# Kernel optimization log

Measured on AMD Instinct MI355X. Metric: run time of the kernel, lower is better.

The kernel has to match this reference:

```python
import jax, jax.numpy as jnp
import numpy as np

B = 16384
DIM = 1024
HEADS = 16
LN_EPS = 1e-5


def setup_inputs() -> dict:
    key = jax.random.key(0)
    ks = jax.random.split(key, 8)
    d = DIM
    s = 0.02
    return {
        "x_u": jax.random.normal(ks[0], (B, d), dtype=jnp.float32),
        "x_m": jax.random.normal(ks[1], (B, d), dtype=jnp.float32),
        # MHA m2u (path 1): packed in_proj [3d, d] like torch, out_proj [d, d]
        "w_qkv1": (jax.random.normal(ks[2], (3 * d, d), dtype=jnp.float32) * s),
        "b_qkv1": jnp.zeros((3 * d,), dtype=jnp.float32),
        "w_o1": (jax.random.normal(ks[3], (d, d), dtype=jnp.float32) * s),
        "b_o1": jnp.zeros((d,), dtype=jnp.float32),
        # MHA u2m (path 2)
        "w_qkv2": (jax.random.normal(ks[4], (3 * d, d), dtype=jnp.float32) * s),
        "b_qkv2": jnp.zeros((3 * d,), dtype=jnp.float32),
        "w_o2": (jax.random.normal(ks[5], (d, d), dtype=jnp.float32) * s),
        "b_o2": jnp.zeros((d,), dtype=jnp.float32),
        # proj head: LayerNorm(2d) + Linear(2d -> d) + GELU (dropout = eval identity)
        "ln_g": jnp.ones((2 * d,), dtype=jnp.float32),
        "ln_b": jnp.zeros((2 * d,), dtype=jnp.float32),
        "w_proj": (jax.random.normal(ks[6], (d, 2 * d), dtype=jnp.float32) * s),
        "b_proj": jnp.zeros((d,), dtype=jnp.float32),
        "heads": HEADS,
    }


def _mha_single_token(xq, xkv, w_qkv, b_qkv, w_o, b_o, heads):
    # seq_len = 1 cross-attention: softmax over a single key is exactly 1.
    d = xq.shape[-1]
    dh = d // heads
    wq, wk, wv = jnp.split(w_qkv, 3, axis=0)
    bq, bk, bv = jnp.split(b_qkv, 3)
    q = (xq @ wq.T + bq).reshape(-1, heads, dh)   # [B, H, dh]
    k = (xkv @ wk.T + bk).reshape(-1, heads, dh)
    v = (xkv @ wv.T + bv).reshape(-1, heads, dh)
    scores = jnp.sum(q * k, axis=-1) / jnp.sqrt(jnp.asarray(dh, q.dtype))  # [B, H]
    attn = jax.nn.softmax(scores[..., None], axis=-1)  # singleton key axis -> ones
    out = (attn * v).reshape(-1, d)                    # [B, d]
    return out @ w_o.T + b_o


def reference(x_u, x_m, w_qkv1, b_qkv1, w_o1, b_o1,
              w_qkv2, b_qkv2, w_o2, b_o2,
              ln_g, ln_b, w_proj, b_proj, heads):
    # Path 1: Q = x_m, K/V = x_u ; Path 2: Q = x_u, K/V = x_m
    z1 = _mha_single_token(x_m, x_u, w_qkv1, b_qkv1, w_o1, b_o1, heads)
    z2 = _mha_single_token(x_u, x_m, w_qkv2, b_qkv2, w_o2, b_o2, heads)
    z = jnp.concatenate([z1, z2], axis=-1)  # [B, 2d]
    mu = jnp.mean(z, axis=-1, keepdims=True)
    var = jnp.mean(jnp.square(z - mu), axis=-1, keepdims=True)
    zn = (z - mu) * jax.lax.rsqrt(var + LN_EPS) * ln_g + ln_b
    h = zn @ w_proj.T + b_proj               # [B, d]
    return jax.nn.gelu(h, approximate=False)  # torch nn.GELU default = exact erf
```

## Files before the change

kernel.cpp:

```cpp
#include <hip/hip_runtime.h>
#include <cstdint>


#define DIM 1024
#define BROWS 16384

typedef __bf16 bf16x8 __attribute__((ext_vector_type(8)));
typedef float f32x4 __attribute__((ext_vector_type(4)));

__device__ __forceinline__ ushort f2bf(float f) {
    uint32_t u = __builtin_bit_cast(uint32_t, f);
    u = (u + 0x7fffu + ((u >> 16) & 1u)) >> 16;
    return (ushort)u;
}

__device__ __forceinline__ void async_copy16(const void* gsrc, void* ldst) {
    __builtin_amdgcn_global_load_lds(
        (__attribute__((address_space(1))) void*)((uintptr_t)gsrc),
        (__attribute__((address_space(3))) void*)((uint32_t)(uintptr_t)ldst),
        16, 0, 0);
}


__global__ __launch_bounds__(256) void prep_kernel(
        const float* __restrict__ x_u, const float* __restrict__ x_m,
        const float* __restrict__ wqkv1, const float* __restrict__ bqkv1,
        const float* __restrict__ wo1, const float* __restrict__ bo1,
        const float* __restrict__ wqkv2, const float* __restrict__ bqkv2,
        const float* __restrict__ wo2, const float* __restrict__ bo2,
        const float* __restrict__ lng, const float* __restrict__ lnb,
        const float* __restrict__ wproj, const float* __restrict__ bproj,
        ushort* __restrict__ x_bf, ushort* __restrict__ wo12,
        ushort* __restrict__ wvT12, ushort* __restrict__ Wp,
        float* __restrict__ b12, float* __restrict__ Svec, float* __restrict__ Cvec,
        float* __restrict__ sums ) {
    const int b = blockIdx.x, t = threadIdx.x;
    __shared__ float red[4][4];
    __shared__ float tls[32][33];

    if (b < 8192) {
        const int n4 = (BROWS * DIM) / 4;
        int i = b * 256 + t;
        const int stride = 8192 * 256;
        const float4* xu4 = (const float4*)x_u;
        const float4* xm4 = (const float4*)x_m;
        ushort4* o4 = (ushort4*)x_bf;
#pragma unroll
        for (int it = 0; it < 4; it++, i += stride) {
            float4 v = (i < n4) ? xu4[i] : xm4[i - n4];
            ushort4 o;
            o.x = f2bf(v.x); o.y = f2bf(v.y); o.z = f2bf(v.z); o.w = f2bf(v.w);
            o4[i] = o;
        }
    } else if (b < 9216) {
        int j = b - 8192;
        float s1 = 0.f, s2 = 0.f, sS = 0.f, sC = 0.f;
        for (int c = t; c < DIM; c += 256) {
            s1 += wo1[j * DIM + c] * bqkv1[2 * DIM + c];
            s2 += wo2[j * DIM + c] * bqkv2[2 * DIM + c];
        }
        for (int c = t; c < 2 * DIM; c += 256) {
            float w = wproj[j * 2 * DIM + c];
            sS += w * lng[c];
            sC += w * lnb[c];
        }
        for (int o = 32; o; o >>= 1) {
            s1 += __shfl_down(s1, o, 64);
            s2 += __shfl_down(s2, o, 64);
            sS += __shfl_down(sS, o, 64);
            sC += __shfl_down(sC, o, 64);
        }
        int wid = t >> 6;
        if ((t & 63) == 0) { red[wid][0] = s1; red[wid][1] = s2; red[wid][2] = sS; red[wid][3] = sC; }
        __syncthreads();
        if (t == 0) {
            s1 = red[0][0] + red[1][0] + red[2][0] + red[3][0];
            s2 = red[0][1] + red[1][1] + red[2][1] + red[3][1];
            sS = red[0][2] + red[1][2] + red[2][2] + red[3][2];
            sC = red[0][3] + red[1][3] + red[2][3] + red[3][3];
            b12[j]       = s1 + bo1[j];
            b12[DIM + j] = s2 + bo2[j];
            Svec[j] = sS;
            Cvec[j] = sC + bproj[j];
        }
    } else if (b < 12288) {
        const int NWO = (DIM * DIM) / 4;
        const int NWP = (DIM * 2 * DIM) / 4;
        const int total = 2 * NWO + NWP;
        int i = (b - 9216) * 256 + t;
        const int stride = 3072 * 256;
        for (; i < total; i += stride) {
            if (i < 2 * NWO) {
                float4 v = (i < NWO) ? ((const float4*)wo1)[i] : ((const float4*)wo2)[i - NWO];
                ushort4 o;
                o.x = f2bf(v.x); o.y = f2bf(v.y); o.z = f2bf(v.z); o.w = f2bf(v.w);
                ((ushort4*)wo12)[i] = o;
            } else {
                int j = i - 2 * NWO;
                float4 v = ((const float4*)wproj)[j];
                int c = (j * 4) & (2 * DIM - 1);
                v.x *= lng[c]; v.y *= lng[c + 1]; v.z *= lng[c + 2]; v.w *= lng[c + 3];
                ushort4 o;
                o.x = f2bf(v.x); o.y = f2bf(v.y); o.z = f2bf(v.z); o.w = f2bf(v.w);
                ((ushort4*)Wp)[j] = o;
            }
        }
    } else if (b < 14336) {
        int tile = b - 12288;
        int z = tile >> 10;
        int t2 = tile & 1023;
        int mt = t2 >> 5, kt = t2 & 31;
        const float* src = z ? wqkv2 : wqkv1;
        int tr = t >> 3;
        int tc4 = (t & 7) * 4;
        const float* p = src + (long)(2 * DIM + mt * 32 + tr) * DIM + kt * 32 + tc4;
        float4 v = *(const float4*)p;
        tls[tr][tc4 + 0] = v.x; tls[tr][tc4 + 1] = v.y;
        tls[tr][tc4 + 2] = v.z; tls[tr][tc4 + 3] = v.w;
        __syncthreads();
        ushort4 o;
        o.x = f2bf(tls[tc4 + 0][tr]);
        o.y = f2bf(tls[tc4 + 1][tr]);
        o.z = f2bf(tls[tc4 + 2][tr]);
        o.w = f2bf(tls[tc4 + 3][tr]);
        *(ushort4*)(wvT12 + (long)z * DIM * DIM + (long)(kt * 32 + tr) * DIM + mt * 32 + tc4) = o;
    } else {
        int i = (b - 14336) * 256 + t;
        ((float4*)sums)[i] = float4{0.f, 0.f, 0.f, 0.f};
    }
}

template <int BM, int BN, int MODE>
__global__ __launch_bounds__(256, 2) void gemm_bt(
        const ushort* __restrict__ Ag, const ushort* __restrict__ Wg,
        void* __restrict__ Cg, int K, int lda, int ldw, int ldc,
        long sAz, long sWz, long sCz,
        const float* __restrict__ bias,
        const float* __restrict__ Svec, const float* __restrict__ Cvec,
        float* __restrict__ sumbuf, float* __restrict__ sqbuf) {
    constexpr int BK = 32;
    constexpr int MT = BM / 32;
    constexpr int NT = BN / 32;
    __shared__ __align__(16) ushort As[BM * BK];
    __shared__ __align__(16) ushort Bs[BN * BK];
    const int tid = threadIdx.x;
    const int wid = tid >> 6;
    const int lane = tid & 63;
    const int quad = lane >> 4;
    const int l16 = lane & 15;
    const int waveM = wid >> 1, waveN = wid & 1;
    const int zb = blockIdx.z;

    const ushort* A = Ag + zb * sAz + (long)blockIdx.x * BM * lda;
    const ushort* W = Wg + zb * sWz + (long)blockIdx.y * BN * ldw;

    f32x4 acc[MT][NT] = {};

    constexpr int nA = (BM * BK) / (256 * 8);
    constexpr int nB = (BN * BK) / (256 * 8);

    const int swz = (l16 >> 1) & 3;
    const int rdA = quad ^ swz;
    for (int k0 = 0; k0 < K; k0 += BK) {
#pragma unroll
        for (int c = 0; c < nA; c++) {
            int idx = c * 256 + tid;
            int r = idx >> 2;
            int q = (idx & 3) ^ ((r >> 1) & 3);
            const ushort* g = A + (long)r * lda + k0 + q * 8;
            async_copy16(g, (char*)As + (c * 256 + wid * 64) * 16);
        }
#pragma unroll
        for (int c = 0; c < nB; c++) {
            int idx = c * 256 + tid;
            int r = idx >> 2;
            int q = (idx & 3) ^ ((r >> 1) & 3);
            const ushort* g = W + (long)r * ldw + k0 + q * 8;
            async_copy16(g, (char*)Bs + (c * 256 + wid * 64) * 16);
        }
        asm volatile("s_waitcnt vmcnt(0)" ::: "memory");
        __syncthreads();

        bf16x8 af[MT], bfg[NT];
#pragma unroll
        for (int im = 0; im < MT; im++)
            af[im] = *(const bf16x8*)(As + (waveM * (BM / 2) + im * 16 + l16) * BK + rdA * 8);
#pragma unroll
        for (int in = 0; in < NT; in++)
            bfg[in] = *(const bf16x8*)(Bs + (waveN * (BN / 2) + in * 16 + l16) * BK + rdA * 8);
#pragma unroll
        for (int im = 0; im < MT; im++)
#pragma unroll
            for (int in = 0; in < NT; in++)
                acc[im][in] = __builtin_amdgcn_mfma_f32_16x16x32_bf16(
                    af[im], bfg[in], acc[im][in], 0, 0, 0);
        __syncthreads();
    }

    const int gRow0 = blockIdx.x * BM + waveM * (BM / 2) + quad * 4;
    const int gCol0 = blockIdx.y * BN + waveN * (BN / 2) + l16;
    if constexpr (MODE == 0) {
        ushort* C = (ushort*)Cg + zb * sCz;
#pragma unroll
        for (int im = 0; im < MT; im++)
#pragma unroll
            for (int in = 0; in < NT; in++) {
                int col = gCol0 + in * 16;
#pragma unroll
                for (int r = 0; r < 4; r++) {
                    int row = gRow0 + im * 16 + r;
                    C[(long)row * ldc + col] = f2bf(acc[im][in][r]);
                }
            }
    } else if constexpr (MODE == 1) {
        ushort* C = (ushort*)Cg + zb * sCz;
        float rs[MT][4] = {};
        float rq[MT][4] = {};
#pragma unroll
        for (int im = 0; im < MT; im++)
#pragma unroll
            for (int in = 0; in < NT; in++) {
                int col = gCol0 + in * 16;
                float badd = bias[zb * DIM + col];
#pragma unroll
                for (int r = 0; r < 4; r++) {
                    int row = gRow0 + im * 16 + r;
                    float val = acc[im][in][r] + badd;
                    C[(long)row * ldc + col] = f2bf(val);
                    rs[im][r] += val;
                    rq[im][r] += val * val;
                }
            }
#pragma unroll
        for (int im = 0; im < MT; im++)
#pragma unroll
            for (int r = 0; r < 4; r++) {
                float s = rs[im][r], q = rq[im][r];
#pragma unroll
                for (int o = 1; o < 16; o <<= 1) {
                    s += __shfl_xor(s, o, 64);
                    q += __shfl_xor(q, o, 64);
                }
                if (l16 == 0) {
                    int row = gRow0 + im * 16 + r;
                    atomicAdd(&sumbuf[row], s);
                    atomicAdd(&sqbuf[row], q);
                }
            }
    } else {
        float* O = (float*)Cg;
#pragma unroll
        for (int im = 0; im < MT; im++)
#pragma unroll
            for (int r = 0; r < 4; r++) {
                int row = gRow0 + im * 16 + r;
                float sv = sumbuf[row], qv = sqbuf[row];
                float m = sv * (1.f / 2048.f);
                float var = qv * (1.f / 2048.f) - m * m;
                float rstd = rsqrtf(var + 1e-5f);
#pragma unroll
                for (int in = 0; in < NT; in++) {
                    int col = gCol0 + in * 16;
                    float h = rstd * (acc[im][in][r] - m * Svec[col]) + Cvec[col];
                    O[(long)row * ldc + col] = 0.5f * h * (1.0f + erff(h * 0.7071067811865475f));
                }
            }
    }
}


extern "C" void kernel_launch(void* const* d_in, const int* in_sizes, int n_in,
                              void* d_out, int out_size, void* d_ws, size_t ws_size,
                              hipStream_t stream) {
    (void)in_sizes; (void)n_in; (void)out_size; (void)ws_size;
    const float* x_u   = (const float*)d_in[0];
    const float* x_m   = (const float*)d_in[1];
    const float* wqkv1 = (const float*)d_in[2];
    const float* bqkv1 = (const float*)d_in[3];
    const float* wo1   = (const float*)d_in[4];
    const float* bo1   = (const float*)d_in[5];
    const float* wqkv2 = (const float*)d_in[6];
    const float* bqkv2 = (const float*)d_in[7];
    const float* wo2   = (const float*)d_in[8];
    const float* bo2   = (const float*)d_in[9];
    const float* lng   = (const float*)d_in[10];
    const float* lnb   = (const float*)d_in[11];
    const float* wproj = (const float*)d_in[12];
    const float* bproj = (const float*)d_in[13];

    char* ws = (char*)d_ws;
    ushort* x_bf  = (ushort*)(ws + 0);
    ushort* wo12  = (ushort*)(ws + 67108864);
    ushort* wvT12 = (ushort*)(ws + 71303168);
    ushort* W12   = (ushort*)(ws + 75497472);
    ushort* Wp    = (ushort*)(ws + 79691776);
    ushort* zbuf  = (ushort*)(ws + 83886080);
    float*  b12   = (float*)(ws + 150994944);
    float*  Svec  = (float*)(ws + 151003136);
    float*  Cvec  = (float*)(ws + 151007232);
    float*  sumbuf= (float*)(ws + 151011328);
    float*  sqbuf = (float*)(ws + 151076864);

    prep_kernel<<<14368, 256, 0, stream>>>(
        x_u, x_m, wqkv1, bqkv1, wo1, bo1, wqkv2, bqkv2, wo2, bo2,
        lng, lnb, wproj, bproj,
        x_bf, wo12, wvT12, Wp, b12, Svec, Cvec, sumbuf);

    gemm_bt<64, 64, 0><<<dim3(16, 16, 2), 256, 0, stream>>>(
        wo12, wvT12, W12, DIM, DIM, DIM, DIM,
        (long)DIM * DIM, (long)DIM * DIM, (long)DIM * DIM,
        nullptr, nullptr, nullptr, nullptr, nullptr);

    gemm_bt<128, 128, 1><<<dim3(128, 8, 2), 256, 0, stream>>>(
        x_bf, W12, zbuf, DIM, DIM, DIM, 2 * DIM,
        (long)BROWS * DIM, (long)DIM * DIM, (long)DIM,
        b12, nullptr, nullptr, sumbuf, sqbuf);

    gemm_bt<128, 128, 2><<<dim3(128, 8, 1), 256, 0, stream>>>(
        zbuf, Wp, d_out, 2 * DIM, 2 * DIM, 2 * DIM, DIM,
        0, 0, 0,
        nullptr, Svec, Cvec, sumbuf, sqbuf);
}
```

Baseline: 408.0 us.

## Use 256x256 tiled GEMM with 4-stage async LDS pipeline for main GEMMs

Replaces the 128x128 single-buffered GEMM for the two big matmuls with a 512-thread 256x256 tile kernel. It uses a 4-deep LDS ring buffer filled by async global-to-LDS copies, with partial vmcnt waits, so loads overlap MFMA compute. It also adds s_setprio around the MFMA bursts. The larger tile raises data reuse per block but uses 128KB of LDS and many accumulator registers, which limits occupancy. The grid also shrinks to 512 blocks, which may leave some CUs idle in the tail.

```diff
diff --git a/kernel.cpp b/kernel.cpp
--- a/kernel.cpp
+++ b/kernel.cpp
@@ -20,7 +20,6 @@
         (__attribute__((address_space(3))) void*)((uint32_t)(uintptr_t)ldst),
         16, 0, 0);
 }
-
 
 __global__ __launch_bounds__(256) void prep_kernel(
         const float* __restrict__ x_u, const float* __restrict__ x_m,
@@ -33,7 +32,7 @@
         ushort* __restrict__ x_bf, ushort* __restrict__ wo12,
         ushort* __restrict__ wvT12, ushort* __restrict__ Wp,
         float* __restrict__ b12, float* __restrict__ Svec, float* __restrict__ Cvec,
-        float* __restrict__ sums ) {
+        float* __restrict__ sums) {
     const int b = blockIdx.x, t = threadIdx.x;
     __shared__ float red[4][4];
     __shared__ float tls[32][33];
@@ -130,15 +129,11 @@
     }
 }
 
-template <int BM, int BN, int MODE>
-__global__ __launch_bounds__(256, 2) void gemm_bt(
+__global__ __launch_bounds__(256, 2) void gemm_w(
         const ushort* __restrict__ Ag, const ushort* __restrict__ Wg,
-        void* __restrict__ Cg, int K, int lda, int ldw, int ldc,
-        long sAz, long sWz, long sCz,
-        const float* __restrict__ bias,
-        const float* __restrict__ Svec, const float* __restrict__ Cvec,
-        float* __restrict__ sumbuf, float* __restrict__ sqbuf) {
-    constexpr int BK = 32;
+        ushort* __restrict__ Cg, int K, int lda, int ldw, int ldc,
+        long sAz, long sWz, long sCz) {
+    constexpr int BM = 64, BN = 64, BK = 32;
     constexpr int MT = BM / 32;
     constexpr int NT = BN / 32;
     __shared__ __align__(16) ushort As[BM * BK];
@@ -155,10 +150,8 @@
     const ushort* W = Wg + zb * sWz + (long)blockIdx.y * BN * ldw;
 
     f32x4 acc[MT][NT] = {};
-
     constexpr int nA = (BM * BK) / (256 * 8);
     constexpr int nB = (BN * BK) / (256 * 8);
-
     const int swz = (l16 >> 1) & 3;
     const int rdA = quad ^ swz;
     for (int k0 = 0; k0 < K; k0 += BK) {
@@ -167,16 +160,14 @@
             int idx = c * 256 + tid;
             int r = idx >> 2;
             int q = (idx & 3) ^ ((r >> 1) & 3);
-            const ushort* g = A + (long)r * lda + k0 + q * 8;
-            async_copy16(g, (char*)As + (c * 256 + wid * 64) * 16);
+            async_copy16(A + (long)r * lda + k0 + q * 8, (char*)As + (c * 256 + wid * 64) * 16);
         }
 #pragma unroll
         for (int c = 0; c < nB; c++) {
             int idx = c * 256 + tid;
             int r = idx >> 2;
             int q = (idx & 3) ^ ((r >> 1) & 3);
-            const ushort* g = W + (long)r * ldw + k0 + q * 8;
-            async_copy16(g, (char*)Bs + (c * 256 + wid * 64) * 16);
+            async_copy16(W + (long)r * ldw + k0 + q * 8, (char*)Bs + (c * 256 + wid * 64) * 16);
         }
         asm volatile("s_waitcnt vmcnt(0)" ::: "memory");
         __syncthreads();
@@ -199,43 +190,159 @@
 
     const int gRow0 = blockIdx.x * BM + waveM * (BM / 2) + quad * 4;
     const int gCol0 = blockIdx.y * BN + waveN * (BN / 2) + l16;
-    if constexpr (MODE == 0) {
+    ushort* C = Cg + zb * sCz;
+#pragma unroll
+    for (int im = 0; im < MT; im++)
+#pragma unroll
+        for (int in = 0; in < NT; in++) {
+            int col = gCol0 + in * 16;
+#pragma unroll
+            for (int r = 0; r < 4; r++) {
+                int row = gRow0 + im * 16 + r;
+                C[(long)row * ldc + col] = f2bf(acc[im][in][r]);
+            }
+        }
+}
+
+template <int MODE>
+__global__ __launch_bounds__(512, 2) void gemm256(
+        const ushort* __restrict__ Ag, const ushort* __restrict__ Wg,
+        void* __restrict__ Cg, int K, int lda, int ldw, int ldc,
+        long sAz, long sWz, long sCz,
+        const float* __restrict__ bias,
+        const float* __restrict__ Svec, const float* __restrict__ Cvec,
+        float* __restrict__ sumbuf, float* __restrict__ sqbuf) {
+    __shared__ __align__(16) ushort As[4 * 8192];
+    __shared__ __align__(16) ushort Bs[4 * 8192];
+    const int tid = threadIdx.x;
+    const int wid = tid >> 6;
+    const int lane = tid & 63;
+    const int quad = lane >> 4;
+    const int l16 = lane & 15;
+    const int waveM = wid >> 2;
+    const int waveN = wid & 3;
+    const int zb = blockIdx.z;
+    const int rd = quad ^ ((l16 >> 1) & 3);
+
+    const ushort* A = Ag + zb * sAz + (long)blockIdx.x * 256 * lda;
+    const ushort* W = Wg + zb * sWz + (long)blockIdx.y * 256 * ldw;
+    const int NTK = K >> 5;
+
+    f32x4 acc[8][4] = {};
+
+#pragma unroll
+    for (int u = 0; u < 3; ++u) {
+        const int k0 = u << 5;
+        char* sa = (char*)As + u * 16384;
+        char* sb = (char*)Bs + u * 16384;
+#pragma unroll
+        for (int rnd = 0; rnd < 2; ++rnd) {
+            int idx = rnd * 512 + tid;
+            int r = idx >> 2;
+            int q = (idx & 3) ^ ((r >> 1) & 3);
+            async_copy16(A + (long)r * lda + k0 + q * 8, sa + (rnd * 512 + wid * 64) * 16);
+        }
+#pragma unroll
+        for (int rnd = 0; rnd < 2; ++rnd) {
+            int idx = rnd * 512 + tid;
+            int r = idx >> 2;
+            int q = (idx & 3) ^ ((r >> 1) & 3);
+            async_copy16(W + (long)r * ldw + k0 + q * 8, sb + (rnd * 512 + wid * 64) * 16);
+        }
+    }
+    asm volatile("s_waitcnt vmcnt(8)" ::: "memory");
+    __builtin_amdgcn_s_barrier();
+    asm volatile("" ::: "memory");
+
+    for (int t = 0; t < NTK; ++t) {
+        const ushort* as = As + (t & 3) * 8192;
+        const ushort* bs = Bs + (t & 3) * 8192;
+        const int u = t + 3;
+        const bool doStage = (u < NTK);
+        char* sa = (char*)As + (u & 3) * 16384;
+        char* sb = (char*)Bs + (u & 3) * 16384;
+        const int k0u = u << 5;
+
+        bf16x8 af[4], bfg[4];
+#pragma unroll
+        for (int j = 0; j < 4; ++j)
+            bfg[j] = *(const bf16x8*)(bs + (waveN * 64 + j * 16 + l16) * 32 + rd * 8);
+#pragma unroll
+        for (int i = 0; i < 4; ++i)
+            af[i] = *(const bf16x8*)(as + (waveM * 128 + i * 16 + l16) * 32 + rd * 8);
+        if (doStage) {
+#pragma unroll
+            for (int rnd = 0; rnd < 2; ++rnd) {
+                int idx = rnd * 512 + tid;
+                int r = idx >> 2;
+                int q = (idx & 3) ^ ((r >> 1) & 3);
+                async_copy16(A + (long)r * lda + k0u + q * 8, sa + (rnd * 512 + wid * 64) * 16);
+            }
+        }
+        __builtin_amdgcn_s_setprio(1);
+#pragma unroll
+        for (int i = 0; i < 4; ++i)
+#pragma unroll
+            for (int j = 0; j < 4; ++j)
+                acc[i][j] = __builtin_amdgcn_mfma_f32_16x16x32_bf16(
+                    af[i], bfg[j], acc[i][j], 0, 0, 0);
+        __builtin_amdgcn_s_setprio(0);
+
+#pragma unroll
+        for (int i = 0; i < 4; ++i)
+            af[i] = *(const bf16x8*)(as + (waveM * 128 + 64 + i * 16 + l16) * 32 + rd * 8);
+        if (doStage) {
+#pragma unroll
+            for (int rnd = 0; rnd < 2; ++rnd) {
+                int idx = rnd * 512 + tid;
+                int r = idx >> 2;
+                int q = (idx & 3) ^ ((r >> 1) & 3);
+                async_copy16(W + (long)r * ldw + k0u + q * 8, sb + (rnd * 512 + wid * 64) * 16);
+            }
+        }
+        __builtin_amdgcn_s_setprio(1);
+#pragma unroll
+        for (int i = 0; i < 4; ++i)
+#pragma unroll
+            for (int j = 0; j < 4; ++j)
+                acc[4 + i][j] = __builtin_amdgcn_mfma_f32_16x16x32_bf16(
+                    af[i], bfg[j], acc[4 + i][j], 0, 0, 0);
+        __builtin_amdgcn_s_setprio(0);
+
+        if (t < NTK - 1) {
+            const int rem = NTK - 1 - t;
+            if (rem >= 3)      asm volatile("s_waitcnt vmcnt(8)" ::: "memory");
+            else if (rem == 2) asm volatile("s_waitcnt vmcnt(4)" ::: "memory");
+            else               asm volatile("s_waitcnt vmcnt(0)" ::: "memory");
+            __builtin_amdgcn_s_barrier();
+            asm volatile("" ::: "memory");
+        }
+    }
+
+    const int gRow0 = blockIdx.x * 256 + waveM * 128 + quad * 4;
+    const int gCol0 = blockIdx.y * 256 + waveN * 64 + l16;
+    if constexpr (MODE == 1) {
         ushort* C = (ushort*)Cg + zb * sCz;
 #pragma unroll
-        for (int im = 0; im < MT; im++)
-#pragma unroll
-            for (int in = 0; in < NT; in++) {
-                int col = gCol0 + in * 16;
-#pragma unroll
-                for (int r = 0; r < 4; r++) {
-                    int row = gRow0 + im * 16 + r;
-                    C[(long)row * ldc + col] = f2bf(acc[im][in][r]);
-                }
-            }
-    } else if constexpr (MODE == 1) {
-        ushort* C = (ushort*)Cg + zb * sCz;
-        float rs[MT][4] = {};
-        float rq[MT][4] = {};
-#pragma unroll
-        for (int im = 0; im < MT; im++)
-#pragma unroll
-            for (int in = 0; in < NT; in++) {
+        for (int im = 0; im < 8; ++im) {
+            float sr[4] = {0.f, 0.f, 0.f, 0.f};
+            float qr[4] = {0.f, 0.f, 0.f, 0.f};
+#pragma unroll
+            for (int in = 0; in < 4; ++in) {
                 int col = gCol0 + in * 16;
                 float badd = bias[zb * DIM + col];
 #pragma unroll
-                for (int r = 0; r < 4; r++) {
+                for (int r = 0; r < 4; ++r) {
                     int row = gRow0 + im * 16 + r;
                     float val = acc[im][in][r] + badd;
                     C[(long)row * ldc + col] = f2bf(val);
-                    rs[im][r] += val;
-                    rq[im][r] += val * val;
+                    sr[r] += val;
+                    qr[r] += val * val;
                 }
             }
 #pragma unroll
-        for (int im = 0; im < MT; im++)
-#pragma unroll
-            for (int r = 0; r < 4; r++) {
-                float s = rs[im][r], q = rq[im][r];
+            for (int r = 0; r < 4; ++r) {
+                float s = sr[r], q = qr[r];
 #pragma unroll
                 for (int o = 1; o < 16; o <<= 1) {
                     s += __shfl_xor(s, o, 64);
@@ -247,24 +354,26 @@
                     atomicAdd(&sqbuf[row], q);
                 }
             }
+        }
     } else {
         float* O = (float*)Cg;
 #pragma unroll
-        for (int im = 0; im < MT; im++)
-#pragma unroll
-            for (int r = 0; r < 4; r++) {
+        for (int im = 0; im < 8; ++im) {
+#pragma unroll
+            for (int r = 0; r < 4; ++r) {
                 int row = gRow0 + im * 16 + r;
                 float sv = sumbuf[row], qv = sqbuf[row];
                 float m = sv * (1.f / 2048.f);
                 float var = qv * (1.f / 2048.f) - m * m;
                 float rstd = rsqrtf(var + 1e-5f);
 #pragma unroll
-                for (int in = 0; in < NT; in++) {
+                for (int in = 0; in < 4; ++in) {
                     int col = gCol0 + in * 16;
                     float h = rstd * (acc[im][in][r] - m * Svec[col]) + Cvec[col];
                     O[(long)row * ldc + col] = 0.5f * h * (1.0f + erff(h * 0.7071067811865475f));
                 }
             }
+        }
     }
 }
 
@@ -306,17 +415,16 @@
         lng, lnb, wproj, bproj,
         x_bf, wo12, wvT12, Wp, b12, Svec, Cvec, sumbuf);
 
-    gemm_bt<64, 64, 0><<<dim3(16, 16, 2), 256, 0, stream>>>(
+    gemm_w<<<dim3(16, 16, 2), 256, 0, stream>>>(
         wo12, wvT12, W12, DIM, DIM, DIM, DIM,
-        (long)DIM * DIM, (long)DIM * DIM, (long)DIM * DIM,
-        nullptr, nullptr, nullptr, nullptr, nullptr);
-
-    gemm_bt<128, 128, 1><<<dim3(128, 8, 2), 256, 0, stream>>>(
+        (long)DIM * DIM, (long)DIM * DIM, (long)DIM * DIM);
+
+    gemm256<1><<<dim3(64, 4, 2), 512, 0, stream>>>(
         x_bf, W12, zbuf, DIM, DIM, DIM, 2 * DIM,
         (long)BROWS * DIM, (long)DIM * DIM, (long)DIM,
         b12, nullptr, nullptr, sumbuf, sqbuf);
 
-    gemm_bt<128, 128, 2><<<dim3(128, 8, 1), 256, 0, stream>>>(
+    gemm256<2><<<dim3(64, 4, 1), 512, 0, stream>>>(
         zbuf, Wp, d_out, 2 * DIM, 2 * DIM, 2 * DIM, DIM,
         0, 0, 0,
         nullptr, Svec, Cvec, sumbuf, sqbuf);
```

Result: faster. 397.0 us (-2.7%).
